# Performance work log

Hardware: AMD Instinct MI355X
Metric: run time of the kernel (lower is better)

Reference implementation:

```python
import jax, jax.numpy as jnp
import numpy as np

B, N, J = 2, 2048, 2048
DIM, HEADS, DH = 1024, 16, 64
INNER = HEADS * DH          # 1024
FF_INNER = 4 * DIM          # 4096
EPS = 1e-5


def layernorm(x, g, b):
    mu = jnp.mean(x, axis=-1, keepdims=True)
    var = jnp.var(x, axis=-1, keepdims=True)
    return (x - mu) * jax.lax.rsqrt(var + EPS) * g + b


def setup_inputs() -> dict:
    key = jax.random.key(0)
    ks = jax.random.split(key, 8)
    s = 0.02
    return {
        "x": jax.random.normal(ks[0], (B, N, DIM), jnp.float32),
        "context": jax.random.normal(ks[1], (B, J, DIM), jnp.float32),
        "norm_g": jnp.ones((DIM,), jnp.float32),
        "norm_b": jnp.zeros((DIM,), jnp.float32),
        "cnorm_g": jnp.ones((DIM,), jnp.float32),
        "cnorm_b": jnp.zeros((DIM,), jnp.float32),
        "Wq": jax.random.normal(ks[2], (DIM, INNER), jnp.float32) * s,
        "Wkv": jax.random.normal(ks[3], (DIM, 2 * DH), jnp.float32) * s,
        "Wo": jax.random.normal(ks[4], (INNER, DIM), jnp.float32) * s,
        "Wff1": jax.random.normal(ks[5], (DIM, 2 * FF_INNER), jnp.float32) * s,
        "Wff2": jax.random.normal(ks[6], (FF_INNER, DIM), jnp.float32) * s,
    }


def reference(x, context, norm_g, norm_b, cnorm_g, cnorm_b, Wq, Wkv, Wo, Wff1, Wff2):
    scale = DH ** -0.5
    xn = layernorm(x, norm_g, norm_b)                      # [b, n, dim]
    cn = layernorm(context, cnorm_g, cnorm_b)              # [b, j, dim]

    q = (xn @ Wq).reshape(B, N, HEADS, DH) * scale         # [b, n, h, dh]
    kv = cn @ Wkv                                          # [b, j, 2*dh]
    k, v = kv[..., :DH], kv[..., DH:]                      # shared across heads (MQA)

    sim = jnp.einsum('bihd,bjd->bhij', q, k)               # [b, h, n, j]
    attn = jax.nn.softmax(sim, axis=-1)                    # amax-stabilized internally
    out = jnp.einsum('bhij,bjd->bihd', attn, v)            # [b, n, h, dh]
    out = out.reshape(B, N, INNER) @ Wo                    # [b, n, dim]

    # parallel SwiGLU FF on the normed input, residual-added
    ff = xn @ Wff1                                         # [b, n, 2*ff_inner]
    a, gate = ff[..., :FF_INNER], ff[..., FF_INNER:]
    out = out + (jax.nn.silu(gate) * a) @ Wff2
    return out
```

## Files before the change

kernel.cpp:

```cpp
#include <hip/hip_runtime.h>
#include <stdint.h>

typedef unsigned short u16;
typedef __attribute__((ext_vector_type(8))) short short8;
typedef __attribute__((ext_vector_type(4))) float f32x4;
typedef __attribute__((ext_vector_type(16))) float f32x16;

#define GPTR(p) ((const __attribute__((address_space(1))) void*)(p))
#define SPTR(p) ((__attribute__((address_space(3))) void*)(p))
#define GLDS16(g, l) __builtin_amdgcn_global_load_lds(GPTR(g), SPTR(l), 16, 0, 0)

static __device__ __forceinline__ float bf2f(u16 u) {
  union { unsigned int i; float f; } c; c.i = ((unsigned int)u) << 16; return c.f;
}
static __device__ __forceinline__ u16 f2bf(float f) {
  union { float f; unsigned int u; } c; c.f = f;
  unsigned int r = 0x7fffu + ((c.u >> 16) & 1u);
  return (u16)((c.u + r) >> 16);
}
static __device__ __forceinline__ unsigned cvtpk(float a, float b) {
  unsigned r;
  asm volatile("v_cvt_pk_bf16_f32 %0, %1, %2" : "=v"(r) : "v"(a), "v"(b));
  return r;
}
static __device__ __forceinline__ int swz4(int row, int c) { return c ^ ((row >> 1) & 3); }

__global__ __launch_bounds__(256) void ln_kernel(
    const float* __restrict__ x, const float* __restrict__ ctx,
    const float* __restrict__ g, const float* __restrict__ b,
    const float* __restrict__ cg, const float* __restrict__ cb,
    u16* __restrict__ xn, u16* __restrict__ cn)
{
  const int row = blockIdx.x;
  const float* src; const float* gg; const float* bb; u16* dst;
  if (row < 4096) { src = x + (size_t)row * 1024; gg = g;  bb = b;  dst = xn + (size_t)row * 1024; }
  else            { src = ctx + (size_t)(row - 4096) * 1024; gg = cg; bb = cb; dst = cn + (size_t)(row - 4096) * 1024; }
  const int t = threadIdx.x;
  float4 v = *(const float4*)&src[t * 4];
  float s  = v.x + v.y + v.z + v.w;
  float s2 = v.x * v.x + v.y * v.y + v.z * v.z + v.w * v.w;
  #pragma unroll
  for (int off = 1; off < 64; off <<= 1) { s += __shfl_xor(s, off); s2 += __shfl_xor(s2, off); }
  __shared__ float ls[4], ls2[4];
  const int w = t >> 6;
  if ((t & 63) == 0) { ls[w] = s; ls2[w] = s2; }
  __syncthreads();
  s  = ls[0] + ls[1] + ls[2] + ls[3];
  s2 = ls2[0] + ls2[1] + ls2[2] + ls2[3];
  const float mu   = s * (1.0f / 1024.0f);
  const float var  = s2 * (1.0f / 1024.0f) - mu * mu;
  const float rstd = rsqrtf(var + 1e-5f);
  float xv[4] = { v.x, v.y, v.z, v.w };
  u16 o[4];
  #pragma unroll
  for (int i = 0; i < 4; ++i)
    o[i] = f2bf((xv[i] - mu) * rstd * gg[t * 4 + i] + bb[t * 4 + i]);
  uint2 pv;
  pv.x = (unsigned)o[0] | ((unsigned)o[1] << 16);
  pv.y = (unsigned)o[2] | ((unsigned)o[3] << 16);
  *(uint2*)&dst[t * 4] = pv;
}

__global__ __launch_bounds__(256) void transpose_k(
    const float* __restrict__ in, u16* __restrict__ out, int R, int C, int ldo, float scale)
{
  __shared__ float tile[64][65];
  const int c0 = blockIdx.x * 64, r0 = blockIdx.y * 64;
  const int t = threadIdx.x;
  const int tr = t >> 4, tc = (t & 15) * 4;
  #pragma unroll
  for (int i = 0; i < 4; ++i) {
    int r = tr + i * 16;
    float4 v = *(const float4*)&in[(size_t)(r0 + r) * C + c0 + tc];
    tile[r][tc + 0] = v.x; tile[r][tc + 1] = v.y; tile[r][tc + 2] = v.z; tile[r][tc + 3] = v.w;
  }
  __syncthreads();
  #pragma unroll
  for (int i = 0; i < 2; ++i) {
    int c  = (t >> 3) + i * 32;
    int rb = (t & 7) * 8;
    union { u16 s[8]; uint4 v; } pk;
    #pragma unroll
    for (int u = 0; u < 8; ++u) pk.s[u] = f2bf(tile[rb + u][c] * scale);
    *(uint4*)&out[(size_t)(c0 + c) * ldo + r0 + rb] = pk.v;
  }
}

__global__ __launch_bounds__(256) void transpose_ff1(
    const float* __restrict__ in, u16* __restrict__ out)
{
  __shared__ float tile[64][65];
  const int c0 = blockIdx.x * 64, r0 = blockIdx.y * 64;
  const int t = threadIdx.x;
  const int tr = t >> 4, tc = (t & 15) * 4;
  #pragma unroll
  for (int i = 0; i < 4; ++i) {
    int r = tr + i * 16;
    float4 v = *(const float4*)&in[(size_t)(r0 + r) * 8192 + c0 + tc];
    tile[r][tc + 0] = v.x; tile[r][tc + 1] = v.y; tile[r][tc + 2] = v.z; tile[r][tc + 3] = v.w;
  }
  __syncthreads();
  #pragma unroll
  for (int i = 0; i < 2; ++i) {
    int c  = (t >> 3) + i * 32;
    int rb = (t & 7) * 8;
    const int gc = c0 + c;
    int j, add16;
    if (gc < 4096) { j = gc; add16 = 0; } else { j = gc - 4096; add16 = 16; }
    const int row = 1024 + ((j >> 7) << 8) + (((j >> 5) & 3) << 6) + (((j >> 4) & 1) << 5) + add16 + (j & 15);
    union { u16 s[8]; uint4 v; } pk;
    #pragma unroll
    for (int u = 0; u < 8; ++u) pk.s[u] = f2bf(tile[rb + u][c]);
    *(uint4*)&out[(size_t)row * 1024 + r0 + rb] = pk.v;
  }
}

#define MM1(MQ, M, NN, BF) acc[MQ][M][NN] = __builtin_amdgcn_mfma_f32_16x16x32_bf16(af##M, BF, acc[MQ][M][NN], 0, 0, 0)
#define MFMA16(MQ, KS) \
  MM1(MQ,0,0,bf##KS##0); MM1(MQ,0,1,bf##KS##1); MM1(MQ,0,2,bf##KS##2); MM1(MQ,0,3,bf##KS##3); \
  MM1(MQ,1,0,bf##KS##0); MM1(MQ,1,1,bf##KS##1); MM1(MQ,1,2,bf##KS##2); MM1(MQ,1,3,bf##KS##3); \
  MM1(MQ,2,0,bf##KS##0); MM1(MQ,2,1,bf##KS##1); MM1(MQ,2,2,bf##KS##2); MM1(MQ,2,3,bf##KS##3); \
  MM1(MQ,3,0,bf##KS##0); MM1(MQ,3,1,bf##KS##1); MM1(MQ,3,2,bf##KS##2); MM1(MQ,3,3,bf##KS##3)

#define SG_A(SBUF, H, KT) do { \
    GLDS16(gA[H][0] + ((size_t)(KT) << 6), SBUF + ((H) * 64 + w16o) * 64); \
    GLDS16(gA[H][1] + ((size_t)(KT) << 6), SBUF + ((H) * 64 + w16o + 8) * 64); \
  } while (0)
#define SG_B(SBUF, H, KT) do { \
    GLDS16(gB[H][0] + ((size_t)(KT) << 6), SBUF + ((H) * 128 + w16o2) * 64); \
    GLDS16(gB[H][1] + ((size_t)(KT) << 6), SBUF + ((H) * 128 + w16o2 + 8) * 64); \
  } while (0)

#define DS_B(PB_) do { \
  bf00 = *(const short8*)(PB_ + 0    + cks0); bf01 = *(const short8*)(PB_ + 1024 + cks0); \
  bf02 = *(const short8*)(PB_ + 2048 + cks0); bf03 = *(const short8*)(PB_ + 3072 + cks0); \
  bf10 = *(const short8*)(PB_ + 0    + cks1); bf11 = *(const short8*)(PB_ + 1024 + cks1); \
  bf12 = *(const short8*)(PB_ + 2048 + cks1); bf13 = *(const short8*)(PB_ + 3072 + cks1); \
} while (0)

#define P_CORE(PA_, MQ, KS, STAGE_STMT, PREB_STMT, GATE_STMT) do { \
  af0 = *(const short8*)(PA_ + (MQ) * 4096 + 0    + cks##KS); \
  af1 = *(const short8*)(PA_ + (MQ) * 4096 + 1024 + cks##KS); \
  af2 = *(const short8*)(PA_ + (MQ) * 4096 + 2048 + cks##KS); \
  af3 = *(const short8*)(PA_ + (MQ) * 4096 + 3072 + cks##KS); \
  STAGE_STMT; \
  PREB_STMT; \
  __builtin_amdgcn_s_barrier(); \
  asm volatile("s_waitcnt lgkmcnt(0)" ::: "memory"); \
  __builtin_amdgcn_s_setprio(1); \
  MFMA16(MQ, KS); \
  __builtin_amdgcn_s_setprio(0); \
  GATE_STMT; \
  __builtin_amdgcn_s_barrier(); \
} while (0)

#define GATE6 asm volatile("s_waitcnt vmcnt(6)" ::: "memory")
#define GATE0 asm volatile("s_waitcnt vmcnt(0)" ::: "memory")
#define HINT8 asm volatile("s_waitcnt lgkmcnt(8)" ::: "memory")

template<int MODE, int ORDER>
__global__ __launch_bounds__(512, 2) void gemm8p(
    const u16* __restrict__ A, const u16* __restrict__ BT, void* __restrict__ C,
    void* __restrict__ C2, int M, int N, int Ktot, int Kslice)
{
  __shared__ u16 sh[2][2][16384];
  const int nbn = N >> 8, nbm = M >> 8;
  const int nwg = gridDim.x;
  const int bid = blockIdx.x;
  const int o = (bid & 7) * (nwg >> 3) + (bid >> 3);
  int bm, bn;
  if constexpr (ORDER == 0) { bm = o % nbm; bn = o / nbm; }
  else                      { bn = o % nbn; bm = o / nbn; }
  const int kbase = blockIdx.y * Kslice;
  const int NI = Kslice >> 7;

  const int t = threadIdx.x, w = t >> 6, lane = t & 63;
  const int wr = w >> 2, wc = w & 3;
  const int lr = lane & 15, lg = lane >> 4;
  const int r8 = lane >> 3, ch = lane & 7;
  const int clog = ch ^ r8;
  const int w16o  = w * 16 + ((w >= 4) ? 64 : 0);
  const int w16o2 = w * 16;

  const u16* gA[2][2]; const u16* gB[2][2];
  #pragma unroll
  for (int h = 0; h < 2; ++h)
    #pragma unroll
    for (int qq = 0; qq < 2; ++qq) {
      gA[h][qq] = A  + (size_t)(bm * 256 + h * 64  + w16o  + qq * 8 + r8) * Ktot + kbase + clog * 8;
      gB[h][qq] = BT + (size_t)(bn * 256 + h * 128 + w16o2 + qq * 8 + r8) * Ktot + kbase + clog * 8;
    }
  u16* sA0 = &sh[0][0][0]; u16* sA1 = &sh[1][0][0];
  u16* sB0 = &sh[0][1][0]; u16* sB1 = &sh[1][1][0];
  const int cks0 = ((0 + lg) ^ (lr & 7)) * 8;
  const int cks1 = ((4 + lg) ^ (lr & 7)) * 8;
  const u16* pA_b0 = sA0 + (wr * 128 + lr) * 64;
  const u16* pA_b1 = sA1 + (wr * 128 + lr) * 64;
  const u16* pB_b0 = sB0 + (wc * 64 + lr) * 64;
  const u16* pB_b1 = sB1 + (wc * 64 + lr) * 64;

  f32x4 acc[2][4][4];
  const f32x4 z4 = { 0.f, 0.f, 0.f, 0.f };
  #pragma unroll
  for (int a = 0; a < 2; ++a)
    #pragma unroll
    for (int b = 0; b < 4; ++b)
      #pragma unroll
      for (int c = 0; c < 4; ++c) acc[a][b][c] = z4;
  short8 af0, af1, af2, af3;
  short8 bf00, bf01, bf02, bf03, bf10, bf11, bf12, bf13;

  SG_B(sB0, 0, 0); SG_B(sB0, 1, 0); SG_A(sA0, 0, 0); SG_A(sA0, 1, 0);
  SG_B(sB1, 0, 1); SG_B(sB1, 1, 1); SG_A(sA1, 0, 1);
  GATE6;
  __builtin_amdgcn_s_barrier();

  for (int i = 0; i < NI; ++i) {
    const int k2 = 2 * i;
    const bool st = (i < NI - 1);
    DS_B(pB_b0);
    P_CORE(pA_b0, 0, 0, SG_A(sA1, 1, k2 + 1), HINT8, );
    P_CORE(pA_b0, 1, 0, if (st) SG_B(sB0, 0, k2 + 2), , );
    P_CORE(pA_b0, 0, 1, if (st) SG_B(sB0, 1, k2 + 2), , );
    P_CORE(pA_b0, 1, 1, if (st) SG_A(sA0, 0, k2 + 2), ,
           if (st) { GATE6; } else { GATE0; });
    DS_B(pB_b1);
    P_CORE(pA_b1, 0, 0, if (st) SG_A(sA0, 1, k2 + 2), HINT8, );
    P_CORE(pA_b1, 1, 0, if (st) SG_B(sB1, 0, k2 + 3), , );
    P_CORE(pA_b1, 0, 1, if (st) SG_B(sB1, 1, k2 + 3), , );
    P_CORE(pA_b1, 1, 1, if (st) SG_A(sA1, 0, k2 + 3), ,
           if (st) { GATE6; });
  }

  if constexpr (MODE == 3) {
    u16* Co = (u16*)C + (size_t)blockIdx.y * M * N;
    #pragma unroll
    for (int mq = 0; mq < 2; ++mq)
      #pragma unroll
      for (int m = 0; m < 4; ++m)
        #pragma unroll
        for (int n = 0; n < 4; ++n)
          #pragma unroll
          for (int rr = 0; rr < 4; ++rr) {
            const int row = bm * 256 + wr * 128 + mq * 64 + m * 16 + lg * 4 + rr;
            const int col = bn * 256 + wc * 64 + n * 16 + lr;
            Co[(size_t)row * N + col] = f2bf(acc[mq][m][n][rr]);
          }
  } else {
    if (bn < 4) {
      u16* Co = (u16*)C;
      #pragma unroll
      for (int mq = 0; mq < 2; ++mq)
        #pragma unroll
        for (int m = 0; m < 4; ++m)
          #pragma unroll
          for (int n = 0; n < 4; ++n)
            #pragma unroll
            for (int rr = 0; rr < 4; ++rr) {
              const int row = bm * 256 + wr * 128 + mq * 64 + m * 16 + lg * 4 + rr;
              const int col = bn * 256 + wc * 64 + n * 16 + lr;
              Co[(size_t)row * 1024 + col] = f2bf(acc[mq][m][n][rr]);
            }
    } else {
      u16* Ho = (u16*)C2;
      const int colb = 1024 + (bn - 4) * 128 + wc * 32 + lr;
      #pragma unroll
      for (int mq = 0; mq < 2; ++mq)
        #pragma unroll
        for (int m = 0; m < 4; ++m)
          #pragma unroll
          for (int rr = 0; rr < 4; ++rr) {
            const int row = bm * 256 + wr * 128 + mq * 64 + m * 16 + lg * 4 + rr;
            #pragma unroll
            for (int n2 = 0; n2 < 2; ++n2) {
              const float a = acc[mq][m][2 * n2][rr];
              const float gt = acc[mq][m][2 * n2 + 1][rr];
              const float h = a * gt / (1.0f + __expf(-gt));
              Ho[(size_t)row * 5120 + colb + n2 * 16] = f2bf(h);
            }
          }
    }
  }
}

__global__ __launch_bounds__(256) void gemm_bt_sk(
    const u16* __restrict__ A, const u16* __restrict__ BT, u16* __restrict__ Cp,
    int M, int N, int Kslice, int Ktot)
{
  __shared__ u16 As[128 * 32];
  __shared__ u16 Bs[128 * 32];
  const int bm = blockIdx.y, bn = blockIdx.x, z = blockIdx.z;
  const int t = threadIdx.x;
  const int w = t >> 6, lane = t & 63;
  const int wr = w >> 1, wc = w & 1;
  const int lr = lane & 15, lkc = lane >> 4;

  f32x4 acc[4][4];
  const f32x4 z4 = { 0.f, 0.f, 0.f, 0.f };
  #pragma unroll
  for (int mi = 0; mi < 4; ++mi)
    #pragma unroll
    for (int ni = 0; ni < 4; ++ni) acc[mi][ni] = z4;

  const int kbase = z * Kslice;
  const int i0 = t, i1 = t + 256;
  const int r0 = i0 >> 2, k0 = swz4(r0, i0 & 3) * 8;
  const int r1 = i1 >> 2, k1 = swz4(r1, i1 & 3) * 8;
  const u16* a0 = A + (size_t)(bm * 128 + r0) * Ktot + kbase + k0;
  const u16* a1 = A + (size_t)(bm * 128 + r1) * Ktot + kbase + k1;
  const u16* b0 = BT + (size_t)(bn * 128 + r0) * Ktot + kbase + k0;
  const u16* b1 = BT + (size_t)(bn * 128 + r1) * Ktot + kbase + k1;
  u16* As0 = As + (size_t)w * 512;
  u16* As1 = As + (size_t)(w + 4) * 512;
  u16* Bs0 = Bs + (size_t)w * 512;
  u16* Bs1 = Bs + (size_t)(w + 4) * 512;

  const int nk = Kslice >> 5;
  for (int kt = 0; kt < nk; ++kt) {
    __syncthreads();
    GLDS16(a0, As0); GLDS16(a1, As1); GLDS16(b0, Bs0); GLDS16(b1, Bs1);
    a0 += 32; a1 += 32; b0 += 32; b1 += 32;
    __syncthreads();
    short8 af[4], bf[4];
    #pragma unroll
    for (int mi = 0; mi < 4; ++mi) {
      int row = wr * 64 + mi * 16 + lr;
      af[mi] = *(const short8*)&As[row * 32 + swz4(row, lkc) * 8];
    }
    #pragma unroll
    for (int ni = 0; ni < 4; ++ni) {
      int row = wc * 64 + ni * 16 + lr;
      bf[ni] = *(const short8*)&Bs[row * 32 + swz4(row, lkc) * 8];
    }
    #pragma unroll
    for (int mi = 0; mi < 4; ++mi)
      #pragma unroll
      for (int ni = 0; ni < 4; ++ni)
        acc[mi][ni] = __builtin_amdgcn_mfma_f32_16x16x32_bf16(af[mi], bf[ni], acc[mi][ni], 0, 0, 0);
  }

  u16* Cz = Cp + (size_t)z * M * N;
  const int row0 = bm * 128 + wr * 64, col0 = bn * 128 + wc * 64;
  const int rsub = (lane >> 4) * 4;
  #pragma unroll
  for (int mi = 0; mi < 4; ++mi)
    #pragma unroll
    for (int ni = 0; ni < 4; ++ni)
      #pragma unroll
      for (int r = 0; r < 4; ++r)
        Cz[(size_t)(row0 + mi * 16 + rsub + r) * N + (col0 + ni * 16 + lr)] = f2bf(acc[mi][ni][r]);
}

__global__ __launch_bounds__(256) void reduce_kv(const u16* __restrict__ part, u16* __restrict__ out)
{
  const size_t base = ((size_t)blockIdx.x * 256 + threadIdx.x) * 8;
  float s[8] = { 0.f, 0.f, 0.f, 0.f, 0.f, 0.f, 0.f, 0.f };
  #pragma unroll
  for (int zz = 0; zz < 8; ++zz) {
    const short8 v = *(const short8*)&part[(size_t)zz * 524288 + base];
    #pragma unroll
    for (int i = 0; i < 8; ++i) s[i] += bf2f((u16)v[i]);
  }
  union { u16 o[8]; uint4 v; } pk;
  #pragma unroll
  for (int i = 0; i < 8; ++i) pk.o[i] = f2bf(s[i]);
  *(uint4*)&out[base] = pk.v;
}

__global__ __launch_bounds__(256) void reduce_out(const u16* __restrict__ part, float* __restrict__ out)
{
  const size_t base = ((size_t)blockIdx.x * 256 + threadIdx.x) * 8;
  float s[8] = { 0.f, 0.f, 0.f, 0.f, 0.f, 0.f, 0.f, 0.f };
  #pragma unroll
  for (int zz = 0; zz < 4; ++zz) {
    const short8 v = *(const short8*)&part[(size_t)zz * 4194304 + base];
    #pragma unroll
    for (int i = 0; i < 8; ++i) s[i] += bf2f((u16)v[i]);
  }
  f32x4 lo = { s[0], s[1], s[2], s[3] };
  f32x4 hi = { s[4], s[5], s[6], s[7] };
  *(f32x4*)&out[base] = lo;
  *(f32x4*)&out[base + 4] = hi;
}

__global__ __launch_bounds__(256) void attn_kernel(
    const u16* __restrict__ q, const u16* __restrict__ kv, u16* __restrict__ o)
{
  __shared__ u16 Ks[128 * 64];
  __shared__ u16 Vt[64 * 128];
  __shared__ u16 Ps[4][32 * 128];
  const int b = blockIdx.z, hb = blockIdx.y, qb = blockIdx.x;
  const int t = threadIdx.x, w = t >> 6, lane = t & 63;
  const int q32 = lane & 31, hl = lane >> 5;
  const int hd = hb * 4 + w;

  const size_t qbase = (size_t)b * 2048 + qb * 64;
  short8 qa[2][4];
  #pragma unroll
  for (int t32 = 0; t32 < 2; ++t32)
    #pragma unroll
    for (int dq = 0; dq < 4; ++dq)
      qa[t32][dq] = *(const short8*)&q[(qbase + t32 * 32 + q32) * 1024 + hd * 64 + dq * 16 + hl * 8];

  f32x16 oacc[2][2];
  #pragma unroll
  for (int i = 0; i < 2; ++i)
    #pragma unroll
    for (int j = 0; j < 2; ++j)
      #pragma unroll
      for (int r = 0; r < 16; ++r) oacc[i][j][r] = 0.f;
  float m_[2] = { -1e30f, -1e30f }, l_[2] = { 0.f, 0.f };

  const size_t kvb = (size_t)b * 2048 * 128;
  const int vd0 = (t & 7) * 8;
  const int vodd = (t >> 3) & 1;
  u16* Pw = &Ps[w][0];

  for (int jt = 0; jt < 16; ++jt) {
    __syncthreads();
    #pragma unroll
    for (int n = 0; n < 4; ++n) {
      const int cc = n * 256 + w * 64;
      const int ccl = cc + lane;
      const int row = ccl >> 3, lc = (ccl & 7) ^ (row & 7);
      GLDS16(&kv[kvb + (size_t)(jt * 128 + row) * 128 + lc * 8], Ks + (size_t)cc * 8);
    }
    #pragma unroll
    for (int c = 0; c < 4; ++c) {
      const int seg = c * 256 + t;
      const int vj = seg >> 3;
      const int jp = vj >> 1;
      const uint4 vv = *(const uint4*)&kv[kvb + (size_t)(jt * 128 + vj) * 128 + 64 + vd0];
      uint4 pvv;
      pvv.x = __shfl_xor((int)vv.x, 8);
      pvv.y = __shfl_xor((int)vv.y, 8);
      pvv.z = __shfl_xor((int)vv.z, 8);
      pvv.w = __shfl_xor((int)vv.w, 8);
      const unsigned ow[4] = { vv.x, vv.y, vv.z, vv.w };
      const unsigned pw[4] = { pvv.x, pvv.y, pvv.z, pvv.w };
      if (!vodd) {
        #pragma unroll
        for (int u = 0; u < 4; ++u) {
          const int d = vd0 + u;
          const unsigned own = (u & 1) ? (ow[u >> 1] >> 16) : (ow[u >> 1] & 0xffffu);
          const unsigned par = (u & 1) ? (pw[u >> 1] >> 16) : (pw[u >> 1] & 0xffffu);
          const int byteoff = d * 256 + ((4 * jp) ^ (((d & 7) ^ ((d >> 3) & 7)) << 4));
          *(unsigned*)((char*)Vt + byteoff) = own | (par << 16);
        }
      } else {
        #pragma unroll
        for (int u = 0; u < 4; ++u) {
          const int ue = u + 4;
          const int d = vd0 + ue;
          const unsigned own = (ue & 1) ? (ow[ue >> 1] >> 16) : (ow[ue >> 1] & 0xffffu);
          const unsigned par = (ue & 1) ? (pw[ue >> 1] >> 16) : (pw[ue >> 1] & 0xffffu);
          const int byteoff = d * 256 + ((4 * jp) ^ (((d & 7) ^ ((d >> 3) & 7)) << 4));
          *(unsigned*)((char*)Vt + byteoff) = par | (own << 16);
        }
      }
    }
    __syncthreads();

    #pragma unroll
    for (int t32 = 0; t32 < 2; ++t32) {
      f32x16 s[4];
      #pragma unroll
      for (int j32 = 0; j32 < 4; ++j32)
        #pragma unroll
        for (int r = 0; r < 16; ++r) s[j32][r] = 0.f;
      #pragma unroll
      for (int j32 = 0; j32 < 4; ++j32) {
        const int row = j32 * 32 + q32;
        #pragma unroll
        for (int dq = 0; dq < 4; ++dq) {
          const int slot = (dq * 2 + hl) ^ (row & 7);
          const short8 kf = *(const short8*)&Ks[row * 64 + slot * 8];
          s[j32] = __builtin_amdgcn_mfma_f32_32x32x16_bf16(kf, qa[t32][dq], s[j32], 0, 0, 0);
        }
      }
      float mt = -1e30f;
      #pragma unroll
      for (int j32 = 0; j32 < 4; ++j32)
        #pragma unroll
        for (int r = 0; r < 16; ++r) mt = fmaxf(mt, s[j32][r]);
      mt = fmaxf(mt, __shfl_xor(mt, 32));
      const bool noresc = (bool)__all(mt <= m_[t32] + 8.0f);
      float nm = m_[t32];
      if (!noresc) {
        nm = fmaxf(m_[t32], mt);
        const float alpha = __expf(m_[t32] - nm);
        m_[t32] = nm;
        l_[t32] *= alpha;
        #pragma unroll
        for (int d32 = 0; d32 < 2; ++d32)
          #pragma unroll
          for (int r = 0; r < 16; ++r) oacc[t32][d32][r] *= alpha;
      }
      float lsum = 0.f;
      #pragma unroll
      for (int j32 = 0; j32 < 4; ++j32) {
        float p[16];
        #pragma unroll
        for (int r = 0; r < 16; ++r) { p[r] = __expf(s[j32][r] - nm); lsum += p[r]; }
        #pragma unroll
        for (int g = 0; g < 4; ++g) {
          const unsigned lo = cvtpk(p[4 * g + 0], p[4 * g + 1]);
          const unsigned hi = cvtpk(p[4 * g + 2], p[4 * g + 3]);
          const int j2 = j32 * 64 + 16 * g + 8 * hl;
          const int byteoff = q32 * 256 + (j2 ^ ((q32 & 7) << 4));
          uint2 wv; wv.x = lo; wv.y = hi;
          *(uint2*)((char*)Pw + byteoff) = wv;
        }
      }
      lsum += __shfl_xor(lsum, 32);
      l_[t32] += lsum;
      short8 pf[8];
      #pragma unroll
      for (int kk = 0; kk < 8; ++kk) {
        const int byteoff = q32 * 256 + ((kk * 32 + hl * 16) ^ ((q32 & 7) << 4));
        pf[kk] = *(const short8*)((const char*)Pw + byteoff);
      }
      #pragma unroll
      for (int d32 = 0; d32 < 2; ++d32) {
        const int dr = d32 * 32 + q32;
        const int vswz = ((dr & 7) ^ ((dr >> 3) & 7)) << 4;
        #pragma unroll
        for (int kk = 0; kk < 8; ++kk) {
          const int byteoff = dr * 256 + ((kk * 32 + hl * 16) ^ vswz);
          const short8 vf = *(const short8*)((const char*)Vt + byteoff);
          oacc[t32][d32] = __builtin_amdgcn_mfma_f32_32x32x16_bf16(vf, pf[kk], oacc[t32][d32], 0, 0, 0);
        }
      }
    }
  }

  float* Ot = (float*)Pw;
  #pragma unroll
  for (int t32 = 0; t32 < 2; ++t32) {
    const float inv = 1.0f / l_[t32];
    #pragma unroll
    for (int d32 = 0; d32 < 2; ++d32) {
      #pragma unroll
      for (int r = 0; r < 16; ++r) {
        const int d = (r & 3) + 8 * (r >> 2) + 4 * hl;
        const int byteoff = q32 * 128 + ((4 * d) ^ ((q32 & 7) << 4));
        *(float*)((char*)Ot + byteoff) = oacc[t32][d32][r] * inv;
      }
      const int qr = lane >> 1, dc = (lane & 1) * 16;
      union { u16 s[16]; uint4 v[2]; } ob;
      #pragma unroll
      for (int cch = 0; cch < 4; ++cch) {
        const int byteoff = qr * 128 + ((4 * (dc + 4 * cch)) ^ ((qr & 7) << 4));
        const f32x4 vv = *(const f32x4*)((const char*)Ot + byteoff);
        ob.s[cch * 4 + 0] = f2bf(vv[0]);
        ob.s[cch * 4 + 1] = f2bf(vv[1]);
        ob.s[cch * 4 + 2] = f2bf(vv[2]);
        ob.s[cch * 4 + 3] = f2bf(vv[3]);
      }
      u16* orow = &o[(qbase + t32 * 32 + qr) * 5120 + hd * 64 + d32 * 32 + dc];
      *(uint4*)orow = ob.v[0];
      *(uint4*)(orow + 8) = ob.v[1];
    }
  }
}

extern "C" void kernel_launch(void* const* d_in, const int* in_sizes, int n_in,
                              void* d_out, int out_size, void* d_ws, size_t ws_size,
                              hipStream_t stream)
{
  const float* x    = (const float*)d_in[0];
  const float* ctx  = (const float*)d_in[1];
  const float* ng   = (const float*)d_in[2];
  const float* nb   = (const float*)d_in[3];
  const float* cg   = (const float*)d_in[4];
  const float* cb   = (const float*)d_in[5];
  const float* Wq   = (const float*)d_in[6];
  const float* Wkv  = (const float*)d_in[7];
  const float* Wo   = (const float*)d_in[8];
  const float* Wff1 = (const float*)d_in[9];
  const float* Wff2 = (const float*)d_in[10];

  u16* p = (u16*)d_ws;
  u16* W1T   = p; p += (size_t)9216 * 1024;
  u16* WkvT  = p; p += (size_t)128 * 1024;
  u16* WcT   = p; p += (size_t)1024 * 5120;
  u16* kvbuf = p; p += (size_t)4096 * 128;
  u16* aoh   = p; p += (size_t)4096 * 5120;
  u16* xn    = p; p += (size_t)4096 * 1024;
  u16* cn    = p; p += (size_t)4096 * 1024;
  u16* qbuf  = p; p += (size_t)4096 * 1024;
  u16* kvpart = W1T;
  u16* ffpart = xn;
  (void)in_sizes; (void)n_in; (void)out_size; (void)ws_size;

  ln_kernel<<<8192, 256, 0, stream>>>(x, ctx, ng, nb, cg, cb, xn, cn);

  transpose_k<<<dim3(16, 16),  256, 0, stream>>>(Wq,   W1T,        1024, 1024, 1024, 0.125f);
  transpose_ff1<<<dim3(128, 16), 256, 0, stream>>>(Wff1, W1T);
  transpose_k<<<dim3(2, 16),   256, 0, stream>>>(Wkv,  WkvT,       1024, 128,  1024, 1.0f);
  transpose_k<<<dim3(16, 16),  256, 0, stream>>>(Wo,   WcT,        1024, 1024, 5120, 1.0f);
  transpose_k<<<dim3(16, 64),  256, 0, stream>>>(Wff2, WcT + 1024, 4096, 1024, 5120, 1.0f);

  gemm8p<2, 0><<<dim3(576), 512, 0, stream>>>(xn, W1T, qbuf, aoh, 4096, 9216, 1024, 1024);
  gemm_bt_sk<<<dim3(1, 32, 8), 256, 0, stream>>>(cn, WkvT, kvpart, 4096, 128, 128, 1024);
  reduce_kv<<<256, 256, 0, stream>>>(kvpart, kvbuf);
  attn_kernel<<<dim3(32, 4, 2), 256, 0, stream>>>(qbuf, kvbuf, aoh);
  gemm8p<3, 1><<<dim3(64, 4), 512, 0, stream>>>(aoh, WcT, ffpart, nullptr, 4096, 1024, 5120, 1280);
  reduce_out<<<2048, 256, 0, stream>>>(ffpart, (float*)d_out);
}
```

Before: 287.5 us.

## Add K=32-step GEMM variant for the fused Q/FF1 projection

Adds a new gemm32 kernel that stages 32-wide K tiles instead of 64, halving LDS use per buffer, with a reworked swizzle, prefetch schedule and vmcnt gating. The first projection GEMM (Q plus SwiGLU FF1) now uses it, while the old kernel is renamed and reduced to the split-K output path. The smaller tile is meant to shorten LDS staging and improve latency hiding, at the cost of twice as many barriers per unit of K.

```diff
diff --git a/kernel.cpp b/kernel.cpp
--- a/kernel.cpp
+++ b/kernel.cpp
@@ -112,6 +112,144 @@
     #pragma unroll
     for (int u = 0; u < 8; ++u) pk.s[u] = f2bf(tile[rb + u][c]);
     *(uint4*)&out[(size_t)row * 1024 + r0 + rb] = pk.v;
+  }
+}
+
+#define MM32(MQ, M, NN) acc[MQ][M][NN] = __builtin_amdgcn_mfma_f32_16x16x32_bf16(af##M, bf##NN, acc[MQ][M][NN], 0, 0, 0)
+#define MFMA16_32(MQ) \
+  MM32(MQ,0,0); MM32(MQ,0,1); MM32(MQ,0,2); MM32(MQ,0,3); \
+  MM32(MQ,1,0); MM32(MQ,1,1); MM32(MQ,1,2); MM32(MQ,1,3); \
+  MM32(MQ,2,0); MM32(MQ,2,1); MM32(MQ,2,2); MM32(MQ,2,3); \
+  MM32(MQ,3,0); MM32(MQ,3,1); MM32(MQ,3,2); MM32(MQ,3,3)
+
+#define SA32(SBUF, H, KT) GLDS16(gA32[H] + ((size_t)(KT) << 5), SBUF + (size_t)((H) * 64 + w16o) * 32)
+#define SB32(SBUF, H, KT) GLDS16(gB32[H] + ((size_t)(KT) << 5), SBUF + (size_t)((H) * 128 + w16o2) * 32)
+
+#define DSB32(PB_) do { \
+  bf0 = *(const short8*)(PB_ + 0    + cks); bf1 = *(const short8*)(PB_ + 512  + cks); \
+  bf2 = *(const short8*)(PB_ + 1024 + cks); bf3 = *(const short8*)(PB_ + 1536 + cks); \
+} while (0)
+
+#define PC32(PA_, MQ, STAGE_STMT, GATE_STMT) do { \
+  af0 = *(const short8*)(PA_ + (MQ) * 2048 + 0    + cks); \
+  af1 = *(const short8*)(PA_ + (MQ) * 2048 + 512  + cks); \
+  af2 = *(const short8*)(PA_ + (MQ) * 2048 + 1024 + cks); \
+  af3 = *(const short8*)(PA_ + (MQ) * 2048 + 1536 + cks); \
+  STAGE_STMT; \
+  __builtin_amdgcn_s_barrier(); \
+  asm volatile("s_waitcnt lgkmcnt(0)" ::: "memory"); \
+  __builtin_amdgcn_s_setprio(1); \
+  MFMA16_32(MQ); \
+  __builtin_amdgcn_s_setprio(0); \
+  GATE_STMT; \
+  __builtin_amdgcn_s_barrier(); \
+} while (0)
+
+#define GATE3 asm volatile("s_waitcnt vmcnt(3)" ::: "memory")
+#define GATE0 asm volatile("s_waitcnt vmcnt(0)" ::: "memory")
+
+template<int MODE, int ORDER>
+__global__ __launch_bounds__(512, 2) void gemm32(
+    const u16* __restrict__ A, const u16* __restrict__ BT, void* __restrict__ C,
+    void* __restrict__ C2, int M, int N, int Ktot, int Kslice)
+{
+  __shared__ u16 sh[2][2][8192];
+  const int nbn = N >> 8, nbm = M >> 8;
+  const int nwg = gridDim.x;
+  const int bid = blockIdx.x;
+  const int o = (bid & 7) * (nwg >> 3) + (bid >> 3);
+  int bm, bn;
+  if constexpr (ORDER == 0) { bm = o % nbm; bn = o / nbm; }
+  else                      { bn = o % nbn; bm = o / nbn; }
+  const int kbase = blockIdx.y * Kslice;
+  const int NI = Kslice >> 6;
+
+  const int t = threadIdx.x, w = t >> 6, lane = t & 63;
+  const int wr = w >> 2, wc = w & 3;
+  const int lr = lane & 15, lg = lane >> 4;
+  const int l4 = lane >> 2, sl = lane & 3;
+  const int w16o  = w * 16 + ((w >= 4) ? 64 : 0);
+  const int w16o2 = w * 16;
+
+  const u16* gA32[2]; const u16* gB32[2];
+  #pragma unroll
+  for (int h = 0; h < 2; ++h) {
+    const int rowA = h * 64 + w16o + l4;
+    gA32[h] = A + (size_t)(bm * 256 + rowA) * Ktot + kbase + (size_t)((sl ^ ((rowA >> 1) & 3)) * 8);
+    const int rowB = h * 128 + w16o2 + l4;
+    gB32[h] = BT + (size_t)(bn * 256 + rowB) * Ktot + kbase + (size_t)((sl ^ ((rowB >> 1) & 3)) * 8);
+  }
+  u16* sA0 = &sh[0][0][0]; u16* sA1 = &sh[1][0][0];
+  u16* sB0 = &sh[0][1][0]; u16* sB1 = &sh[1][1][0];
+  const int cks = (lg ^ ((lr >> 1) & 3)) * 8;
+  const u16* pA_b0 = sA0 + (wr * 128 + lr) * 32;
+  const u16* pA_b1 = sA1 + (wr * 128 + lr) * 32;
+  const u16* pB_b0 = sB0 + (wc * 64 + lr) * 32;
+  const u16* pB_b1 = sB1 + (wc * 64 + lr) * 32;
+
+  f32x4 acc[2][4][4];
+  const f32x4 z4 = { 0.f, 0.f, 0.f, 0.f };
+  #pragma unroll
+  for (int a = 0; a < 2; ++a)
+    #pragma unroll
+    for (int b = 0; b < 4; ++b)
+      #pragma unroll
+      for (int c = 0; c < 4; ++c) acc[a][b][c] = z4;
+  short8 af0, af1, af2, af3;
+  short8 bf0, bf1, bf2, bf3;
+
+  SA32(sA0, 0, 0); SA32(sA0, 1, 0); SB32(sB0, 0, 0); SB32(sB0, 1, 0);
+  SB32(sB1, 0, 1); SB32(sB1, 1, 1); SA32(sA1, 0, 1);
+  GATE3;
+  __builtin_amdgcn_s_barrier();
+
+  for (int i = 0; i < NI; ++i) {
+    const bool st = (i < NI - 1);
+    const int X = 2 * i + 2, Y = 2 * i + 3;
+    DSB32(pB_b0);
+    PC32(pA_b0, 0, SA32(sA1, 1, 2 * i + 1), );
+    PC32(pA_b0, 1,
+         if (st) { SB32(sB0, 0, X); SB32(sB0, 1, X); SA32(sA0, 0, X); },
+         if (st) { GATE3; } else { GATE0; });
+    DSB32(pB_b1);
+    PC32(pA_b1, 0, if (st) { SA32(sA0, 1, X); }, );
+    PC32(pA_b1, 1,
+         if (st) { SB32(sB1, 0, Y); SB32(sB1, 1, Y); SA32(sA1, 0, Y); },
+         if (st) { GATE3; });
+  }
+
+  if (bn < 4) {
+    u16* Co = (u16*)C;
+    #pragma unroll
+    for (int mq = 0; mq < 2; ++mq)
+      #pragma unroll
+      for (int m = 0; m < 4; ++m)
+        #pragma unroll
+        for (int n = 0; n < 4; ++n)
+          #pragma unroll
+          for (int rr = 0; rr < 4; ++rr) {
+            const int row = bm * 256 + wr * 128 + mq * 64 + m * 16 + lg * 4 + rr;
+            const int col = bn * 256 + wc * 64 + n * 16 + lr;
+            Co[(size_t)row * 1024 + col] = f2bf(acc[mq][m][n][rr]);
+          }
+  } else {
+    u16* Ho = (u16*)C2;
+    const int colb = 1024 + (bn - 4) * 128 + wc * 32 + lr;
+    #pragma unroll
+    for (int mq = 0; mq < 2; ++mq)
+      #pragma unroll
+      for (int m = 0; m < 4; ++m)
+        #pragma unroll
+        for (int rr = 0; rr < 4; ++rr) {
+          const int row = bm * 256 + wr * 128 + mq * 64 + m * 16 + lg * 4 + rr;
+          #pragma unroll
+          for (int n2 = 0; n2 < 2; ++n2) {
+            const float a = acc[mq][m][2 * n2][rr];
+            const float gt = acc[mq][m][2 * n2 + 1][rr];
+            const float h = a * gt / (1.0f + __expf(-gt));
+            Ho[(size_t)row * 5120 + colb + n2 * 16] = f2bf(h);
+          }
+        }
   }
 }
 
@@ -155,11 +293,10 @@
 } while (0)
 
 #define GATE6 asm volatile("s_waitcnt vmcnt(6)" ::: "memory")
-#define GATE0 asm volatile("s_waitcnt vmcnt(0)" ::: "memory")
 #define HINT8 asm volatile("s_waitcnt lgkmcnt(8)" ::: "memory")
 
 template<int MODE, int ORDER>
-__global__ __launch_bounds__(512, 2) void gemm8p(
+__global__ __launch_bounds__(512, 2) void gemm64(
     const u16* __restrict__ A, const u16* __restrict__ BT, void* __restrict__ C,
     void* __restrict__ C2, int M, int N, int Ktot, int Kslice)
 {
@@ -232,55 +369,19 @@
            if (st) { GATE6; });
   }
 
-  if constexpr (MODE == 3) {
-    u16* Co = (u16*)C + (size_t)blockIdx.y * M * N;
-    #pragma unroll
-    for (int mq = 0; mq < 2; ++mq)
-      #pragma unroll
-      for (int m = 0; m < 4; ++m)
-        #pragma unroll
-        for (int n = 0; n < 4; ++n)
-          #pragma unroll
-          for (int rr = 0; rr < 4; ++rr) {
-            const int row = bm * 256 + wr * 128 + mq * 64 + m * 16 + lg * 4 + rr;
-            const int col = bn * 256 + wc * 64 + n * 16 + lr;
-            Co[(size_t)row * N + col] = f2bf(acc[mq][m][n][rr]);
-          }
-  } else {
-    if (bn < 4) {
-      u16* Co = (u16*)C;
-      #pragma unroll
-      for (int mq = 0; mq < 2; ++mq)
-        #pragma unroll
-        for (int m = 0; m < 4; ++m)
-          #pragma unroll
-          for (int n = 0; n < 4; ++n)
-            #pragma unroll
-            for (int rr = 0; rr < 4; ++rr) {
-              const int row = bm * 256 + wr * 128 + mq * 64 + m * 16 + lg * 4 + rr;
-              const int col = bn * 256 + wc * 64 + n * 16 + lr;
-              Co[(size_t)row * 1024 + col] = f2bf(acc[mq][m][n][rr]);
-            }
-    } else {
-      u16* Ho = (u16*)C2;
-      const int colb = 1024 + (bn - 4) * 128 + wc * 32 + lr;
-      #pragma unroll
-      for (int mq = 0; mq < 2; ++mq)
-        #pragma unroll
-        for (int m = 0; m < 4; ++m)
-          #pragma unroll
-          for (int rr = 0; rr < 4; ++rr) {
-            const int row = bm * 256 + wr * 128 + mq * 64 + m * 16 + lg * 4 + rr;
-            #pragma unroll
-            for (int n2 = 0; n2 < 2; ++n2) {
-              const float a = acc[mq][m][2 * n2][rr];
-              const float gt = acc[mq][m][2 * n2 + 1][rr];
-              const float h = a * gt / (1.0f + __expf(-gt));
-              Ho[(size_t)row * 5120 + colb + n2 * 16] = f2bf(h);
-            }
-          }
-    }
-  }
+  u16* Co = (u16*)C + (size_t)blockIdx.y * M * N;
+  #pragma unroll
+  for (int mq = 0; mq < 2; ++mq)
+    #pragma unroll
+    for (int m = 0; m < 4; ++m)
+      #pragma unroll
+      for (int n = 0; n < 4; ++n)
+        #pragma unroll
+        for (int rr = 0; rr < 4; ++rr) {
+          const int row = bm * 256 + wr * 128 + mq * 64 + m * 16 + lg * 4 + rr;
+          const int col = bn * 256 + wc * 64 + n * 16 + lr;
+          Co[(size_t)row * N + col] = f2bf(acc[mq][m][n][rr]);
+        }
 }
 
 __global__ __launch_bounds__(256) void gemm_bt_sk(
@@ -601,10 +702,10 @@
   transpose_k<<<dim3(16, 16),  256, 0, stream>>>(Wo,   WcT,        1024, 1024, 5120, 1.0f);
   transpose_k<<<dim3(16, 64),  256, 0, stream>>>(Wff2, WcT + 1024, 4096, 1024, 5120, 1.0f);
 
-  gemm8p<2, 0><<<dim3(576), 512, 0, stream>>>(xn, W1T, qbuf, aoh, 4096, 9216, 1024, 1024);
+  gemm32<2, 0><<<dim3(576), 512, 0, stream>>>(xn, W1T, qbuf, aoh, 4096, 9216, 1024, 1024);
   gemm_bt_sk<<<dim3(1, 32, 8), 256, 0, stream>>>(cn, WkvT, kvpart, 4096, 128, 128, 1024);
   reduce_kv<<<256, 256, 0, stream>>>(kvpart, kvbuf);
   attn_kernel<<<dim3(32, 4, 2), 256, 0, stream>>>(qbuf, kvbuf, aoh);
-  gemm8p<3, 1><<<dim3(64, 4), 512, 0, stream>>>(aoh, WcT, ffpart, nullptr, 4096, 1024, 5120, 1280);
+  gemm64<3, 1><<<dim3(64, 4), 512, 0, stream>>>(aoh, WcT, ffpart, nullptr, 4096, 1024, 5120, 1280);
   reduce_out<<<2048, 256, 0, stream>>>(ffpart, (float*)d_out);
 }
```

After: 289.8 us. Within noise of the previous version (+0.8%).
